# Optimization experiments

Measured on AMD Instinct MI355X. Metric: run time of the kernel, lower is better.

## Reference

```python
import jax, jax.numpy as jnp
import numpy as np

B, IN, H, L = 128, 256, 1024, 256
nA, nB = H // 2, (H - 1) // 2        # pairs per A-layer / B-layer
LB = L // 2
LA = L - LB                           # A layers come first when L is odd
PI = float(np.pi)


def setup_inputs() -> dict:
    key = jax.random.key(0)
    ks = jax.random.split(key, 14)
    u = lambda k, shp: jax.random.uniform(k, shp, minval=-PI, maxval=PI)
    return {
        "inputsR": jax.random.normal(ks[0], (B, IN), dtype=jnp.float32),
        "inputsI": jax.random.normal(ks[1], (B, IN), dtype=jnp.float32),
        "stateR": jax.random.normal(ks[2], (B, H), dtype=jnp.float32),
        "stateI": jax.random.normal(ks[3], (B, H), dtype=jnp.float32),
        # CLinear params (init_scale=0.01 inside RNNCellCmplx)
        "weightR": 0.01 * jax.random.normal(ks[4], (H, IN), dtype=jnp.float32),
        "weightI": 0.01 * jax.random.normal(ks[5], (H, IN), dtype=jnp.float32),
        "biasR": 0.01 * jax.random.normal(ks[6], (H,), dtype=jnp.float32),
        "biasI": 0.01 * jax.random.normal(ks[7], (H,), dtype=jnp.float32),
        # Clements mesh angles, uniform(-pi, pi)
        "angleA0": u(ks[8], (LA, nA)),
        "angleA1": u(ks[9], (LA, nA)),
        "angleB0": u(ks[10], (LB, nB)),
        "angleB1": u(ks[11], (LB, nB)),
        # diagonal phase + modReLU bias (both init to zero)
        "omega": jnp.zeros((H,), dtype=jnp.float32),
        "mod_bias": jnp.zeros((H,), dtype=jnp.float32),
    }


def _mzi(ar, ai, br, bi, th0, th1):
    """PSDC MZI on channel pairs: phase shifter e^{i*th0} on arm a, then a
    directional coupler with coupling angle th1 (unitary 2x2)."""
    c0, s0 = jnp.cos(th0), jnp.sin(th0)
    pr = c0 * ar - s0 * ai          # p = e^{i th0} * a
    pi_ = s0 * ar + c0 * ai
    c, s = jnp.cos(th1), jnp.sin(th1)
    oar = c * pr - s * bi           # a' = cos*p + i sin*b
    oai = c * pi_ + s * br
    obr = c * br - s * pi_          # b' = i sin*p + cos*b
    obi = c * bi + s * pr
    return oar, oai, obr, obi


def _layerA(xr, xi, t0, t1):
    Bs, N = xr.shape
    oar, oai, obr, obi = _mzi(xr[:, 0::2], xi[:, 0::2], xr[:, 1::2], xi[:, 1::2], t0, t1)
    xr = jnp.stack([oar, obr], axis=-1).reshape(Bs, N)
    xi = jnp.stack([oai, obi], axis=-1).reshape(Bs, N)
    return xr, xi


def _layerB(xr, xi, t0, t1):
    Bs, N = xr.shape  # pairs (1,2),(3,4),... ; channels 0 and N-1 pass through
    oar, oai, obr, obi = _mzi(xr[:, 1:-1:2], xi[:, 1:-1:2], xr[:, 2::2], xi[:, 2::2], t0, t1)
    midr = jnp.stack([oar, obr], axis=-1).reshape(Bs, N - 2)
    midi = jnp.stack([oai, obi], axis=-1).reshape(Bs, N - 2)
    xr = jnp.concatenate([xr[:, :1], midr, xr[:, -1:]], axis=1)
    xi = jnp.concatenate([xi[:, :1], midi, xi[:, -1:]], axis=1)
    return xr, xi


def _clements(xr, xi, A0, A1, B0, B1):
    def step(carry, ang):
        cr, ci = carry
        a0, a1, b0, b1 = ang
        cr, ci = _layerA(cr, ci, a0, a1)
        cr, ci = _layerB(cr, ci, b0, b1)
        return (cr, ci), None
    (xr, xi), _ = jax.lax.scan(step, (xr, xi), (A0[:LB], A1[:LB], B0, B1))
    for k in range(LB, LA):  # trailing A layer when num_layers is odd (static)
        xr, xi = _layerA(xr, xi, A0[k], A1[k])
    return xr, xi


def _forward(inputsR, inputsI, stateR, stateI, weightR, weightI, biasR, biasI,
             angleA0, angleA1, angleB0, angleB1, omega, mod_bias):
    # CLinear: complex y = W x + b
    ihR = inputsR @ weightR.T - inputsI @ weightI.T + biasR
    ihI = inputsR @ weightI.T + inputsI @ weightR.T + biasI
    # Clements unitary mesh on hidden state
    hr, hi = _clements(stateR, stateI, angleA0, angleA1, angleB0, angleB1)
    # diagonal phase e^{i omega}
    co, so = jnp.cos(omega), jnp.sin(omega)
    hhR = co * hr - so * hi
    hhI = so * hr + co * hi
    # complex add
    zr = ihR + hhR
    zi = ihI + hhI
    # modReLU: relu(|z| + b) * z / |z|
    mag = jnp.sqrt(zr * zr + zi * zi)
    scale = jax.nn.relu(mag + mod_bias) / jnp.maximum(mag, 1e-8)
    return jnp.stack([scale * zr, scale * zi])  # (2, B, H)


def reference(inputsR, inputsI, stateR, stateI, weightR, weightI, biasR, biasI,
              angleA0, angleA1, angleB0, angleB1, omega, mod_bias):
    return _forward(inputsR, inputsI, stateR, stateI, weightR, weightI, biasR, biasI,
                    angleA0, angleA1, angleB0, angleB1, omega, mod_bias)
```

## Files before the change

### kernel.cpp

```cpp
#include <hip/hip_runtime.h>
#include <math.h>

typedef float v2 __attribute__((ext_vector_type(2)));

#define NBATCH 128
#define NIN    256
#define NH     1024
#define NSTEPS 128
#define NB     511

#define TAB_F4_PER_L 1024
#define IH_OFF (NSTEPS * TAB_F4_PER_L * 4)

#define GEMM_BLOCKS 256
#define TRIG_BLOCKS 512

static __device__ __forceinline__ v2 to2(float a, float b) { v2 r; r.x = a; r.y = b; return r; }

__global__ __launch_bounds__(256) void prep_kernel(
    const float* __restrict__ inR, const float* __restrict__ inI,
    const float* __restrict__ wR,  const float* __restrict__ wI,
    const float* __restrict__ biasR, const float* __restrict__ biasI,
    const float* __restrict__ A0, const float* __restrict__ A1,
    const float* __restrict__ B0, const float* __restrict__ B1,
    float* __restrict__ ws)
{
    __shared__ v2 xs[256][17];
    __shared__ v2 wsh[32][34];

    if (blockIdx.x >= GEMM_BLOCKS) {
        int idx = (blockIdx.x - GEMM_BLOCKS) * 256 + threadIdx.x;
        int l = idx >> 10;
        int s = idx & 1023;
        int j = s >> 8, g = s & 255;
        float a0, a1;
        bool ident = false;
        if (j < 2) {
            int p = 2 * g + j;
            a0 = A0[l * 512 + p]; a1 = A1[l * 512 + p];
        } else {
            int p = 2 * g + (j - 2);
            if (p < NB) { a0 = B0[l * NB + p]; a1 = B1[l * NB + p]; }
            else ident = true;
        }
        float4 v;
        if (ident) v = make_float4(1.f, 0.f, 1.f, 0.f);
        else {
            float s0, c0, s1, c1;
            __sincosf(a0, &s0, &c0);
            __sincosf(a1, &s1, &c1);
            v = make_float4(c0, s0, c1, s1);
        }
        ((float4*)ws)[l * TAB_F4_PER_L + j * 256 + g] = v;
        return;
    }

    const int ht = blockIdx.x >> 3, bt = blockIdx.x & 7;
    const int h0 = ht * 32, b0 = bt * 16;
    const int tid = threadIdx.x;

    {
        int b = tid >> 4, k4 = tid & 15;
#pragma unroll
        for (int p = 0; p < 4; ++p) {
            int k0 = p * 64 + k4 * 4;
            float4 vr = *(const float4*)(inR + (b0 + b) * NIN + k0);
            float4 vi = *(const float4*)(inI + (b0 + b) * NIN + k0);
            xs[k0 + 0][b] = to2(vr.x, vi.x);
            xs[k0 + 1][b] = to2(vr.y, vi.y);
            xs[k0 + 2][b] = to2(vr.z, vi.z);
            xs[k0 + 3][b] = to2(vr.w, vi.w);
        }
    }

    const int hg = tid & 15, bl = tid >> 4;
    v2 acc0 = to2(0.f, 0.f), acc1 = to2(0.f, 0.f);

    for (int c = 0; c < 8; ++c) {
        __syncthreads();
        {
            int hh = tid >> 3, k4 = tid & 7;
            float4 vr = *(const float4*)(wR + (h0 + hh) * NIN + c * 32 + k4 * 4);
            float4 vi = *(const float4*)(wI + (h0 + hh) * NIN + c * 32 + k4 * 4);
            wsh[k4 * 4 + 0][hh] = to2(vr.x, vi.x);
            wsh[k4 * 4 + 1][hh] = to2(vr.y, vi.y);
            wsh[k4 * 4 + 2][hh] = to2(vr.z, vi.z);
            wsh[k4 * 4 + 3][hh] = to2(vr.w, vi.w);
        }
        __syncthreads();
#pragma unroll
        for (int k = 0; k < 32; ++k) {
            float4 wv = *(const float4*)&wsh[k][hg * 2];
            v2 w0 = to2(wv.x, wv.y), w1 = to2(wv.z, wv.w);
            v2 xv = xs[c * 32 + k][bl];
            acc0 += to2(xv.x, xv.x) * w0 + to2(xv.y, xv.y) * to2(-w0.y, w0.x);
            acc1 += to2(xv.x, xv.x) * w1 + to2(xv.y, xv.y) * to2(-w1.y, w1.x);
        }
    }
    int h = h0 + hg * 2, b = b0 + bl;
    acc0 += to2(biasR[h], biasI[h]);
    acc1 += to2(biasR[h + 1], biasI[h + 1]);
    ((float4*)(ws + IH_OFF))[b * 512 + (h >> 1)] =
        make_float4(acc0.x, acc0.y, acc1.x, acc1.y);
}

__device__ __forceinline__ void mzi(const float4 t, v2& a, v2& b)
{
    v2 P  = to2(t.x, t.y) * to2(a.x, a.x) + to2(-t.y, t.x) * to2(a.y, a.y);
    v2 na = to2(t.z, t.z) * P + to2(-t.w, t.w) * to2(b.y, b.x);
    b     = to2(t.z, t.z) * b + to2(-t.w, t.w) * to2(P.y, P.x);
    a = na;
}

__device__ __forceinline__ void stepf(v2 x[4], const float4* T, const float4 TL,
                                      int w, int lane, int par,
                                      v2 (*sx0)[3], v2 (*sx3)[3])
{
    mzi(T[0], x[0], x[1]);
    mzi(T[1], x[2], x[3]);
    if (lane == 0 && w > 0)  sx0[par][w - 1] = x[0];
    if (lane == 63 && w < 3) sx3[par][w] = x[3];
    __asm__ volatile("s_waitcnt lgkmcnt(0)" ::: "memory");
    __builtin_amdgcn_s_barrier();
    __asm__ volatile("" ::: "memory");

    float rcr = __shfl_down(x[0].x, 1, 64);
    float rci = __shfl_down(x[0].y, 1, 64);
    float lcr = __shfl_up(x[3].x, 1, 64);
    float lci = __shfl_up(x[3].y, 1, 64);
    if (lane == 63 && w < 3) { v2 t = sx0[par][w]; rcr = t.x; rci = t.y; }
    if (lane == 0 && w > 0)  { v2 t = sx3[par][w - 1]; lcr = t.x; lci = t.y; }

    mzi(T[2], x[1], x[2]);

    {
        const float4 t = T[3];
        v2 P = to2(t.x, t.y) * to2(x[3].x, x[3].x) + to2(-t.y, t.x) * to2(x[3].y, x[3].y);
        x[3] = to2(t.z, t.z) * P + to2(-t.w, t.w) * to2(rci, rcr);
    }
    {
        v2 P = to2(TL.x, TL.y) * to2(lcr, lcr) + to2(-TL.y, TL.x) * to2(lci, lci);
        x[0] = to2(TL.z, TL.z) * x[0] + to2(-TL.w, TL.w) * to2(P.y, P.x);
    }
}

#define LOADL(T, TL, l)                                                   \
    do {                                                                  \
        const float4* _p = tab + (l) * TAB_F4_PER_L + g;                  \
        T[0] = _p[0];                                                     \
        T[1] = _p[256];                                                   \
        T[2] = _p[512];                                                   \
        T[3] = _p[768];                                                   \
        TL = _p[767];                                     \
        if (g == 0) TL = make_float4(1.f, 0.f, 1.f, 0.f);                 \
    } while (0)

__global__ __launch_bounds__(256, 1) void mesh_kernel(
    const float* __restrict__ stateR, const float* __restrict__ stateI,
    const float* __restrict__ omega,  const float* __restrict__ mod_bias,
    const float* __restrict__ ws, float* __restrict__ out)
{
    const int b = blockIdx.x;
    const int g = threadIdx.x;
    const int lane = g & 63;
    const int w = g >> 6;
    const float4* tab = (const float4*)ws;

    __shared__ v2 sx0[2][3];
    __shared__ v2 sx3[2][3];

    v2 x[4];
    {
        float4 r = *(const float4*)(stateR + b * NH + 4 * g);
        float4 i = *(const float4*)(stateI + b * NH + 4 * g);
        x[0] = to2(r.x, i.x);
        x[1] = to2(r.y, i.y);
        x[2] = to2(r.z, i.z);
        x[3] = to2(r.w, i.w);
    }

    float4 Ta[4], Tb[4], TLa, TLb;
    LOADL(Ta, TLa, 0);
    for (int l = 0; l < NSTEPS; l += 2) {
        LOADL(Tb, TLb, l + 1);
        stepf(x, Ta, TLa, w, lane, 0, sx0, sx3);
        {
            int ln = (l + 2 < NSTEPS) ? l + 2 : NSTEPS - 1;
            LOADL(Ta, TLa, ln);
        }
        stepf(x, Tb, TLb, w, lane, 1, sx0, sx3);
    }

    float4 o4 = *(const float4*)(omega + 4 * g);
    float4 m4 = *(const float4*)(mod_bias + 4 * g);
    const float4* ihp = (const float4*)(ws + IH_OFF) + b * 512 + 2 * g;
    float4 ih0 = ihp[0], ih1 = ihp[1];

    float om[4] = { o4.x, o4.y, o4.z, o4.w };
    float mb[4] = { m4.x, m4.y, m4.z, m4.w };
    float ihr[4] = { ih0.x, ih0.z, ih1.x, ih1.z };
    float ihi[4] = { ih0.y, ih0.w, ih1.y, ih1.w };
    float oR[4], oI[4];
#pragma unroll
    for (int j = 0; j < 4; ++j) {
        float so, co;
        __sincosf(om[j], &so, &co);
        float zr = ihr[j] + co * x[j].x - so * x[j].y;
        float zi = ihi[j] + so * x[j].x + co * x[j].y;
        float mag = sqrtf(zr * zr + zi * zi);
        float sc = fmaxf(mag + mb[j], 0.f) / fmaxf(mag, 1e-8f);
        oR[j] = sc * zr;
        oI[j] = sc * zi;
    }
    *(float4*)(out + b * NH + 4 * g) = make_float4(oR[0], oR[1], oR[2], oR[3]);
    *(float4*)(out + NBATCH * NH + b * NH + 4 * g) = make_float4(oI[0], oI[1], oI[2], oI[3]);
}

extern "C" void kernel_launch(void* const* d_in, const int* in_sizes, int n_in,
                              void* d_out, int out_size, void* d_ws, size_t ws_size,
                              hipStream_t stream)
{
    const float* inputsR = (const float*)d_in[0];
    const float* inputsI = (const float*)d_in[1];
    const float* stateR  = (const float*)d_in[2];
    const float* stateI  = (const float*)d_in[3];
    const float* weightR = (const float*)d_in[4];
    const float* weightI = (const float*)d_in[5];
    const float* biasR   = (const float*)d_in[6];
    const float* biasI   = (const float*)d_in[7];
    const float* angleA0 = (const float*)d_in[8];
    const float* angleA1 = (const float*)d_in[9];
    const float* angleB0 = (const float*)d_in[10];
    const float* angleB1 = (const float*)d_in[11];
    const float* omega   = (const float*)d_in[12];
    const float* mod_b   = (const float*)d_in[13];
    float* ws = (float*)d_ws;
    float* out = (float*)d_out;

    hipLaunchKernelGGL(prep_kernel, dim3(GEMM_BLOCKS + TRIG_BLOCKS), dim3(256),
                       0, stream, inputsR, inputsI, weightR, weightI,
                       biasR, biasI, angleA0, angleA1, angleB0, angleB1, ws);
    hipLaunchKernelGGL(mesh_kernel, dim3(NBATCH), dim3(256), 0, stream,
                       stateR, stateI, omega, mod_b, ws, out);
}
```

Measured before the change: 151.0 us.

## Stage mesh angle tables into LDS via async global_load_lds triple buffer

```diff
diff --git a/kernel.cpp b/kernel.cpp
--- a/kernel.cpp
+++ b/kernel.cpp
@@ -112,48 +112,19 @@
     a = na;
 }
 
-__device__ __forceinline__ void stepf(v2 x[4], const float4* T, const float4 TL,
-                                      int w, int lane, int par,
-                                      v2 (*sx0)[3], v2 (*sx3)[3])
-{
-    mzi(T[0], x[0], x[1]);
-    mzi(T[1], x[2], x[3]);
-    if (lane == 0 && w > 0)  sx0[par][w - 1] = x[0];
-    if (lane == 63 && w < 3) sx3[par][w] = x[3];
-    __asm__ volatile("s_waitcnt lgkmcnt(0)" ::: "memory");
-    __builtin_amdgcn_s_barrier();
-    __asm__ volatile("" ::: "memory");
-
-    float rcr = __shfl_down(x[0].x, 1, 64);
-    float rci = __shfl_down(x[0].y, 1, 64);
-    float lcr = __shfl_up(x[3].x, 1, 64);
-    float lci = __shfl_up(x[3].y, 1, 64);
-    if (lane == 63 && w < 3) { v2 t = sx0[par][w]; rcr = t.x; rci = t.y; }
-    if (lane == 0 && w > 0)  { v2 t = sx3[par][w - 1]; lcr = t.x; lci = t.y; }
-
-    mzi(T[2], x[1], x[2]);
-
-    {
-        const float4 t = T[3];
-        v2 P = to2(t.x, t.y) * to2(x[3].x, x[3].x) + to2(-t.y, t.x) * to2(x[3].y, x[3].y);
-        x[3] = to2(t.z, t.z) * P + to2(-t.w, t.w) * to2(rci, rcr);
-    }
-    {
-        v2 P = to2(TL.x, TL.y) * to2(lcr, lcr) + to2(-TL.y, TL.x) * to2(lci, lci);
-        x[0] = to2(TL.z, TL.z) * x[0] + to2(-TL.w, TL.w) * to2(P.y, P.x);
-    }
-}
-
-#define LOADL(T, TL, l)                                                   \
-    do {                                                                  \
-        const float4* _p = tab + (l) * TAB_F4_PER_L + g;                  \
-        T[0] = _p[0];                                                     \
-        T[1] = _p[256];                                                   \
-        T[2] = _p[512];                                                   \
-        T[3] = _p[768];                                                   \
-        TL = _p[767];                                     \
-        if (g == 0) TL = make_float4(1.f, 0.f, 1.f, 0.f);                 \
-    } while (0)
+__device__ __forceinline__ void stage_layer(const float4* __restrict__ tab, int l,
+                                            float4* dst, int w, int lane)
+{
+    const float4* src = tab + l * TAB_F4_PER_L + w * 256 + lane;
+    float4* d = dst + w * 256;
+#pragma unroll
+    for (int c = 0; c < 4; ++c) {
+        __builtin_amdgcn_global_load_lds(
+            (const __attribute__((address_space(1))) unsigned int*)(src + c * 64),
+            (__attribute__((address_space(3))) unsigned int*)(d + c * 64),
+            16, 0, 0);
+    }
+}
 
 __global__ __launch_bounds__(256, 1) void mesh_kernel(
     const float* __restrict__ stateR, const float* __restrict__ stateI,
@@ -166,6 +137,7 @@
     const int w = g >> 6;
     const float4* tab = (const float4*)ws;
 
+    __shared__ float4 tb[3][TAB_F4_PER_L];
     __shared__ v2 sx0[2][3];
     __shared__ v2 sx3[2][3];
 
@@ -179,16 +151,62 @@
         x[3] = to2(r.w, i.w);
     }
 
-    float4 Ta[4], Tb[4], TLa, TLb;
-    LOADL(Ta, TLa, 0);
-    for (int l = 0; l < NSTEPS; l += 2) {
-        LOADL(Tb, TLb, l + 1);
-        stepf(x, Ta, TLa, w, lane, 0, sx0, sx3);
+    stage_layer(tab, 0, &tb[0][0], w, lane);
+    stage_layer(tab, 1, &tb[1][0], w, lane);
+    __asm__ volatile("s_waitcnt vmcnt(0)" ::: "memory");
+    __syncthreads();
+
+    float4 T0 = tb[0][g], T1 = tb[0][256 + g], T2 = tb[0][512 + g], T3 = tb[0][768 + g];
+    float4 TL = tb[0][768 + ((g - 1) & 255)];
+    if (g == 0) TL = make_float4(1.f, 0.f, 1.f, 0.f);
+
+    int s = 0;
+    for (int l = 0; l < NSTEPS; ++l) {
+        const int par = l & 1;
+        mzi(T0, x[0], x[1]);
+        mzi(T1, x[2], x[3]);
+        if (lane == 0 && w > 0)  sx0[par][w - 1] = x[0];
+        if (lane == 63 && w < 3) sx3[par][w] = x[3];
+        __asm__ volatile("s_waitcnt vmcnt(0) lgkmcnt(0)" ::: "memory");
+        __builtin_amdgcn_s_barrier();
+        __asm__ volatile("" ::: "memory");
+
+        int s2 = s + 2; if (s2 >= 3) s2 -= 3;
+        if (l + 2 < NSTEPS) stage_layer(tab, l + 2, &tb[s2][0], w, lane);
+
+        float rcr = __shfl_down(x[0].x, 1, 64);
+        float rci = __shfl_down(x[0].y, 1, 64);
+        float lcr = __shfl_up(x[3].x, 1, 64);
+        float lci = __shfl_up(x[3].y, 1, 64);
+        if (lane == 63 && w < 3) { v2 t = sx0[par][w]; rcr = t.x; rci = t.y; }
+        if (lane == 0 && w > 0)  { v2 t = sx3[par][w - 1]; lcr = t.x; lci = t.y; }
+
+        mzi(T2, x[1], x[2]);
+
+        int s1 = s + 1; if (s1 >= 3) s1 -= 3;
+        float4 N0, N1, N2, N3, NL;
+        if (l + 1 < NSTEPS) {
+            N0 = tb[s1][g];
+            N1 = tb[s1][256 + g];
+            N2 = tb[s1][512 + g];
+            N3 = tb[s1][768 + g];
+            NL = tb[s1][768 + ((g - 1) & 255)];
+        } else {
+            N0 = N1 = N2 = N3 = NL = make_float4(1.f, 0.f, 1.f, 0.f);
+        }
+
         {
-            int ln = (l + 2 < NSTEPS) ? l + 2 : NSTEPS - 1;
-            LOADL(Ta, TLa, ln);
-        }
-        stepf(x, Tb, TLb, w, lane, 1, sx0, sx3);
+            v2 P = to2(T3.x, T3.y) * to2(x[3].x, x[3].x) + to2(-T3.y, T3.x) * to2(x[3].y, x[3].y);
+            x[3] = to2(T3.z, T3.z) * P + to2(-T3.w, T3.w) * to2(rci, rcr);
+        }
+        {
+            v2 P = to2(TL.x, TL.y) * to2(lcr, lcr) + to2(-TL.y, TL.x) * to2(lci, lci);
+            x[0] = to2(TL.z, TL.z) * x[0] + to2(-TL.w, TL.w) * to2(P.y, P.x);
+        }
+
+        T0 = N0; T1 = N1; T2 = N2; T3 = N3; TL = NL;
+        if (g == 0) TL = make_float4(1.f, 0.f, 1.f, 0.f);
+        s = s1;
     }
 
     float4 o4 = *(const float4*)(omega + 4 * g);
```

New measurement: 181.1 us. 19.9% more time.
